# Kernel optimization log

Measured on AMD Instinct MI355X. Metric: run time of the kernel, lower is better.

The kernel has to match this reference:

```python
import jax, jax.numpy as jnp
import numpy as np

H = 2048
EPS = 1e-5

def _layernorm(x, g, b):
    mu = jnp.mean(x, axis=-1, keepdims=True)
    var = jnp.mean(jnp.square(x - mu), axis=-1, keepdims=True)
    return (x - mu) * jax.lax.rsqrt(var + EPS) * g + b

def setup_inputs() -> dict:
    key = jax.random.key(0)
    ks = jax.random.split(key, 12)
    s = 1.0 / np.sqrt(H)
    inp = {
        "x": jax.random.normal(ks[0], (2, 2048, H), dtype=jnp.float32),
        "ln1_g": jnp.ones((H,), jnp.float32),
        "ln1_b": jnp.zeros((H,), jnp.float32),
        "ln2_g": jnp.ones((H,), jnp.float32),
        "ln2_b": jnp.zeros((H,), jnp.float32),
        "qkv_w": jax.random.uniform(ks[1], (H, 3 * H), jnp.float32, -s, s),
        "qkv_b": jax.random.uniform(ks[2], (3 * H,), jnp.float32, -s, s),
        "out_w": jax.random.uniform(ks[3], (H, H), jnp.float32, -s, s),
        "out_b": jax.random.uniform(ks[4], (H,), jnp.float32, -s, s),
        "mlp_w1": jax.random.uniform(ks[5], (H, 4 * H), jnp.float32, -s, s),
        "mlp_b1": jax.random.uniform(ks[6], (4 * H,), jnp.float32, -s, s),
        "mlp_w2": jax.random.uniform(ks[7], (4 * H, H), jnp.float32, -1.0 / np.sqrt(4 * H), 1.0 / np.sqrt(4 * H)),
        "mlp_b2": jax.random.uniform(ks[8], (H,), jnp.float32, -1.0 / np.sqrt(4 * H), 1.0 / np.sqrt(4 * H)),
    }
    return inp

def reference(x, ln1_g, ln1_b, ln2_g, ln2_b, qkv_w, qkv_b, out_w, out_b, mlp_w1, mlp_b1, mlp_w2, mlp_b2):
    residual = x
    h = _layernorm(x, ln1_g, ln1_b)
    qkv = h @ qkv_w + qkv_b                      # [B,S,3H]
    q, k, v = jnp.split(qkv, 3, axis=-1)         # each [B,S,H] (single-head attention)
    scores = jnp.einsum('bsh,bth->bst', q, k) / jnp.sqrt(jnp.float32(H))
    attn = jax.nn.softmax(scores, axis=-1)
    attn_out = jnp.einsum('bst,bth->bsh', attn, v)
    attn_out = attn_out @ out_w + out_b
    x = residual + attn_out                      # dropout is identity in eval
    residual = x
    h = _layernorm(x, ln2_g, ln2_b)
    h = jax.nn.gelu(h @ mlp_w1 + mlp_b1, approximate=False)
    h = h @ mlp_w2 + mlp_b2
    return residual + h
```

## Files before the change

### kernel.cpp

```cpp
#include <hip/hip_runtime.h>
#include <hip/hip_bf16.h>
#include <math.h>

typedef __bf16 bf16_t;
typedef __bf16 bf16x8 __attribute__((ext_vector_type(8)));
typedef __bf16 bf16x4 __attribute__((ext_vector_type(4)));
typedef float  f32x4  __attribute__((ext_vector_type(4)));

enum { EPI_BF16_BIAS = 0, EPI_F32_SCALE = 1, EPI_BF16 = 2, EPI_F32_BIAS_RES = 3, EPI_BF16_BIAS_GELU = 4 };

__device__ __forceinline__ float gelu_exact(float v) {
  return 0.5f * v * (1.0f + erff(v * 0.7071067811865476f));
}

__device__ __forceinline__ void gld_lds16(const bf16_t* g, bf16_t* l) {
  __builtin_amdgcn_global_load_lds(
      (const __attribute__((address_space(1))) uint32_t*)(uintptr_t)g,
      (__attribute__((address_space(3))) uint32_t*)(uintptr_t)l, 16, 0, 0);
}

#define PH_BARRIER() do { __builtin_amdgcn_s_barrier(); __builtin_amdgcn_sched_barrier(0); } while(0)
#define LGKM0() do { asm volatile("s_waitcnt lgkmcnt(0)" ::: "memory"); __builtin_amdgcn_sched_barrier(0); } while(0)
#define VMCNT4() asm volatile("s_waitcnt vmcnt(4)" ::: "memory")
#define VMCNT0() asm volatile("s_waitcnt vmcnt(0)" ::: "memory")

#define RD(base, rowbase, ks) \
  (*(const bf16x8*)((base) + ((rowbase) + lr) * 64 + (((((ks) << 2) | lg)) ^ (lr & 7)) * 8))

#define DO_MFMA(IBASE, JBASE) \
  __builtin_amdgcn_s_setprio(1); \
  { _Pragma("unroll") for (int ii = 0; ii < 4; ++ii) \
    _Pragma("unroll") for (int jj = 0; jj < 2; ++jj) \
    _Pragma("unroll") for (int ks = 0; ks < 2; ++ks) \
      acc[(IBASE)+ii][(JBASE)+jj] = __builtin_amdgcn_mfma_f32_16x16x32_bf16( \
          aF[ii][ks], bF[jj][ks], acc[(IBASE)+ii][(JBASE)+jj], 0, 0, 0); } \
  __builtin_amdgcn_s_setprio(0);

template<int EPI>
__global__ __launch_bounds__(512, 2) void tb_gemm8(
    const bf16_t* __restrict__ A, int lda, long long strideA,
    const bf16_t* __restrict__ B, int ldb, long long strideB,
    const float* __restrict__ bias,
    const float* __restrict__ resid,
    void* __restrict__ Cp, int ldc, long long strideC,
    int K, float scale)
{
  __shared__ __align__(16) bf16_t sm[65536];

  const int tid = threadIdx.x;
  const int lane = tid & 63;
  const int wid = tid >> 6;
  const int wm = wid >> 2;
  const int wn = wid & 3;
  const int lr = lane & 15;
  const int lg = lane >> 4;
  const int z = blockIdx.z;
  const int m0 = blockIdx.y * 256;
  const int n0 = blockIdx.x * 256;

  const bf16_t* Ag = A + (size_t)z * strideA;
  const bf16_t* Bg = B + (size_t)z * strideB;

  const int l3 = lane >> 3;
  const int sl8 = ((lane & 7) ^ l3) << 3;

  f32x4 acc[8][4];
#pragma unroll
  for (int i = 0; i < 8; ++i)
#pragma unroll
    for (int j = 0; j < 4; ++j) acc[i][j] = (f32x4){0.f, 0.f, 0.f, 0.f};

  auto stage = [&](bf16_t* da, bf16_t* db, int kt, int H) {
#pragma unroll
    for (int q = 0; q < 2; ++q) {
      int c = (wid << 1) + q;
      int row = (H << 7) + (c << 3) + l3;
      gld_lds16(Ag + (size_t)(m0 + row) * lda + kt + sl8, da + (H << 13) + (c << 9) + lane * 8);
      gld_lds16(Bg + (size_t)(n0 + row) * ldb + kt + sl8, db + (H << 13) + (c << 9) + lane * 8);
    }
  };

  const int NT = K >> 6;
  stage(sm, sm + 16384, 0, 0);
  stage(sm, sm + 16384, 0, 1);

  bf16x8 aF[4][2], bF[2][2];

  for (int t = 0; t < NT; ++t) {
    bf16_t* cura = sm + ((t & 1) << 15);
    bf16_t* curb = cura + 16384;
    bf16_t* nxta = sm + (((t + 1) & 1) << 15);
    bf16_t* nxtb = nxta + 16384;
    const int ktn = (t + 1) << 6;
    const bool lastt = (t == NT - 1);

    VMCNT4();
    PH_BARRIER();
#pragma unroll
    for (int ii = 0; ii < 4; ++ii) {
      aF[ii][0] = RD(cura, ii * 32 + wm * 16, 0);
      aF[ii][1] = RD(cura, ii * 32 + wm * 16, 1);
    }
#pragma unroll
    for (int jj = 0; jj < 2; ++jj) {
      bF[jj][0] = RD(curb, jj * 64 + wn * 16, 0);
      bF[jj][1] = RD(curb, jj * 64 + wn * 16, 1);
    }
    if (!lastt) stage(nxta, nxtb, ktn, 0);
    LGKM0();
    DO_MFMA(0, 0);

    if (lastt) { VMCNT0(); } else { VMCNT4(); }
    PH_BARRIER();
#pragma unroll
    for (int jj = 0; jj < 2; ++jj) {
      bF[jj][0] = RD(curb, 128 + jj * 64 + wn * 16, 0);
      bF[jj][1] = RD(curb, 128 + jj * 64 + wn * 16, 1);
    }
    if (!lastt) stage(nxta, nxtb, ktn, 1);
    LGKM0();
    DO_MFMA(0, 2);

    PH_BARRIER();
#pragma unroll
    for (int ii = 0; ii < 4; ++ii) {
      aF[ii][0] = RD(cura, 128 + ii * 32 + wm * 16, 0);
      aF[ii][1] = RD(cura, 128 + ii * 32 + wm * 16, 1);
    }
    LGKM0();
    DO_MFMA(4, 2);

    PH_BARRIER();
#pragma unroll
    for (int jj = 0; jj < 2; ++jj) {
      bF[jj][0] = RD(curb, jj * 64 + wn * 16, 0);
      bF[jj][1] = RD(curb, jj * 64 + wn * 16, 1);
    }
    LGKM0();
    DO_MFMA(4, 0);
  }

#pragma unroll
  for (int i = 0; i < 8; ++i) {
    const int mr = ((i >> 2) << 7) + ((i & 3) << 5) + (wm << 4);
#pragma unroll
    for (int j = 0; j < 4; ++j) {
      const int nc = ((j >> 1) << 7) + ((j & 1) << 6) + (wn << 4);
#pragma unroll
      for (int r = 0; r < 4; ++r) {
        int row = m0 + mr + lg * 4 + r;
        int col = n0 + nc + lr;
        float v = acc[i][j][r] * scale;
        if constexpr (EPI == EPI_BF16_BIAS || EPI == EPI_F32_BIAS_RES || EPI == EPI_BF16_BIAS_GELU)
          v += bias[col];
        if constexpr (EPI == EPI_BF16_BIAS_GELU)
          v = gelu_exact(v);
        if constexpr (EPI == EPI_F32_BIAS_RES)
          v += resid[(size_t)row * ldc + col];
        if constexpr (EPI == EPI_BF16_BIAS || EPI == EPI_BF16 || EPI == EPI_BF16_BIAS_GELU) {
          ((bf16_t*)Cp)[(size_t)z * strideC + (size_t)row * ldc + col] = (bf16_t)v;
        } else {
          ((float*)Cp)[(size_t)z * strideC + (size_t)row * ldc + col] = v;
        }
      }
    }
  }
}

__global__ __launch_bounds__(256) void tb_transpose_cast(
    const float* __restrict__ in, bf16_t* __restrict__ outT, int R, int C)
{
  __shared__ float tile[32][33];
  int c0 = blockIdx.x * 32;
  int r0 = blockIdx.y * 32;
  int t = threadIdx.x;
  int r = t >> 3;
  int c4 = (t & 7) * 4;
  float4 d = *(const float4*)(in + (size_t)(r0 + r) * C + c0 + c4);
  tile[r][c4 + 0] = d.x; tile[r][c4 + 1] = d.y; tile[r][c4 + 2] = d.z; tile[r][c4 + 3] = d.w;
  __syncthreads();
  int c = t >> 3;
  int r4 = (t & 7) * 4;
  bf16x4 o;
  o[0] = (bf16_t)tile[r4 + 0][c];
  o[1] = (bf16_t)tile[r4 + 1][c];
  o[2] = (bf16_t)tile[r4 + 2][c];
  o[3] = (bf16_t)tile[r4 + 3][c];
  *(bf16x4*)(outT + (size_t)(c0 + c) * R + r0 + r4) = o;
}

__global__ __launch_bounds__(256) void tb_transpose_bf16(
    const bf16_t* __restrict__ in, int ldin, long long sIn,
    bf16_t* __restrict__ out, int ldout, long long sOut)
{
  __shared__ bf16_t tile[32][40];
  int z = blockIdx.z;
  const bf16_t* src = in + (size_t)z * sIn;
  bf16_t* dst = out + (size_t)z * sOut;
  int c0 = blockIdx.x * 32;
  int r0 = blockIdx.y * 32;
  int t = threadIdx.x;
  int r = t >> 3;
  int c4 = (t & 7) * 4;
  bf16x4 d = *(const bf16x4*)(src + (size_t)(r0 + r) * ldin + c0 + c4);
  *(bf16x4*)&tile[r][c4] = d;
  __syncthreads();
  int c = t >> 3;
  int r4 = (t & 7) * 4;
  bf16x4 o;
  o[0] = tile[r4 + 0][c];
  o[1] = tile[r4 + 1][c];
  o[2] = tile[r4 + 2][c];
  o[3] = tile[r4 + 3][c];
  *(bf16x4*)(dst + (size_t)(c0 + c) * ldout + r0 + r4) = o;
}

__global__ __launch_bounds__(256) void tb_layernorm(
    const float* __restrict__ x, const float* __restrict__ g, const float* __restrict__ b,
    bf16_t* __restrict__ h)
{
  __shared__ float sa[4], sb[4];
  int row = blockIdx.x;
  int t = threadIdx.x;
  const float* xr = x + (size_t)row * 2048;
  float4 v0 = *(const float4*)(xr + t * 8);
  float4 v1 = *(const float4*)(xr + t * 8 + 4);
  float a[8] = {v0.x, v0.y, v0.z, v0.w, v1.x, v1.y, v1.z, v1.w};
  float s = 0.f, q = 0.f;
#pragma unroll
  for (int j = 0; j < 8; ++j) { s += a[j]; q += a[j] * a[j]; }
#pragma unroll
  for (int o = 32; o; o >>= 1) { s += __shfl_down(s, o); q += __shfl_down(q, o); }
  int w = t >> 6, l = t & 63;
  if (l == 0) { sa[w] = s; sb[w] = q; }
  __syncthreads();
  if (t == 0) {
    sa[0] = sa[0] + sa[1] + sa[2] + sa[3];
    sb[0] = sb[0] + sb[1] + sb[2] + sb[3];
  }
  __syncthreads();
  float mu = sa[0] * (1.0f / 2048.0f);
  float var = sb[0] * (1.0f / 2048.0f) - mu * mu;
  float rs = rsqrtf(var + 1e-5f);
  float4 g0 = *(const float4*)(g + t * 8);
  float4 g1 = *(const float4*)(g + t * 8 + 4);
  float4 b0 = *(const float4*)(b + t * 8);
  float4 b1 = *(const float4*)(b + t * 8 + 4);
  float gv[8] = {g0.x, g0.y, g0.z, g0.w, g1.x, g1.y, g1.z, g1.w};
  float bv[8] = {b0.x, b0.y, b0.z, b0.w, b1.x, b1.y, b1.z, b1.w};
  bf16x8 o8;
#pragma unroll
  for (int j = 0; j < 8; ++j) o8[j] = (bf16_t)((a[j] - mu) * rs * gv[j] + bv[j]);
  *(bf16x8*)(h + (size_t)row * 2048 + t * 8) = o8;
}

__global__ __launch_bounds__(256) void tb_softmax(
    const float* __restrict__ S, bf16_t* __restrict__ P)
{
  __shared__ float sa[4];
  int row = blockIdx.x;
  int t = threadIdx.x;
  const float* sr = S + (size_t)row * 2048;
  float4 a0 = *(const float4*)(sr + t * 8);
  float4 a1 = *(const float4*)(sr + t * 8 + 4);
  float v[8] = {a0.x, a0.y, a0.z, a0.w, a1.x, a1.y, a1.z, a1.w};
  float m = v[0];
#pragma unroll
  for (int j = 1; j < 8; ++j) m = fmaxf(m, v[j]);
#pragma unroll
  for (int o = 32; o; o >>= 1) m = fmaxf(m, __shfl_down(m, o));
  int w = t >> 6, l = t & 63;
  if (l == 0) sa[w] = m;
  __syncthreads();
  if (t == 0) sa[0] = fmaxf(fmaxf(sa[0], sa[1]), fmaxf(sa[2], sa[3]));
  __syncthreads();
  m = sa[0];
  __syncthreads();
  float s = 0.f;
#pragma unroll
  for (int j = 0; j < 8; ++j) { v[j] = expf(v[j] - m); s += v[j]; }
#pragma unroll
  for (int o = 32; o; o >>= 1) s += __shfl_down(s, o);
  if (l == 0) sa[w] = s;
  __syncthreads();
  if (t == 0) sa[0] = sa[0] + sa[1] + sa[2] + sa[3];
  __syncthreads();
  float inv = 1.0f / sa[0];
  bf16x8 o8;
#pragma unroll
  for (int j = 0; j < 8; ++j) o8[j] = (bf16_t)(v[j] * inv);
  *(bf16x8*)(P + (size_t)row * 2048 + t * 8) = o8;
}

extern "C" void kernel_launch(void* const* d_in, const int* in_sizes, int n_in,
                              void* d_out, int out_size, void* d_ws, size_t ws_size,
                              hipStream_t stream) {
  const float* x     = (const float*)d_in[0];
  const float* ln1_g = (const float*)d_in[1];
  const float* ln1_b = (const float*)d_in[2];
  const float* ln2_g = (const float*)d_in[3];
  const float* ln2_b = (const float*)d_in[4];
  const float* qkv_w = (const float*)d_in[5];
  const float* qkv_b = (const float*)d_in[6];
  const float* out_w = (const float*)d_in[7];
  const float* out_b = (const float*)d_in[8];
  const float* w1    = (const float*)d_in[9];
  const float* b1    = (const float*)d_in[10];
  const float* w2    = (const float*)d_in[11];
  const float* b2    = (const float*)d_in[12];
  float* out = (float*)d_out;
  char* ws = (char*)d_ws;

  bf16_t* qkv_wT = (bf16_t*)(ws + 0);
  bf16_t* out_wT = (bf16_t*)(ws + 25165824);
  bf16_t* w1T    = (bf16_t*)(ws + 33554432);
  bf16_t* w2T    = (bf16_t*)(ws + 67108864);
  bf16_t* h_bf   = (bf16_t*)(ws + 100663296);
  bf16_t* qkv_bf = (bf16_t*)(ws + 117440512);
  float*  scores = (float*)(ws + 167772160);
  bf16_t* attn_bf= (bf16_t*)(ws + 201326592);
  bf16_t* ao_bf  = (bf16_t*)(ws + 218103808);
  float*  x2     = (float*)(ws + 234881024);
  bf16_t* mid_bf = (bf16_t*)(ws + 117440512);
  bf16_t* Vt     = (bf16_t*)(ws + 234881024);

  const float inv_sqrt_h = 0.022097086912079608f;

  tb_transpose_cast<<<dim3(6144 / 32, 2048 / 32), 256, 0, stream>>>(qkv_w, qkv_wT, 2048, 6144);
  tb_transpose_cast<<<dim3(2048 / 32, 2048 / 32), 256, 0, stream>>>(out_w, out_wT, 2048, 2048);
  tb_transpose_cast<<<dim3(8192 / 32, 2048 / 32), 256, 0, stream>>>(w1, w1T, 2048, 8192);
  tb_transpose_cast<<<dim3(2048 / 32, 8192 / 32), 256, 0, stream>>>(w2, w2T, 8192, 2048);

  tb_layernorm<<<4096, 256, 0, stream>>>(x, ln1_g, ln1_b, h_bf);

  tb_gemm8<EPI_BF16_BIAS><<<dim3(24, 16, 1), 512, 0, stream>>>(
      h_bf, 2048, 0, qkv_wT, 2048, 0, qkv_b, nullptr, qkv_bf, 6144, 0, 2048, 1.0f);

  tb_transpose_bf16<<<dim3(64, 64, 2), 256, 0, stream>>>(
      qkv_bf + 4096, 6144, 2048LL * 6144, Vt, 2048, 2048LL * 2048);

  tb_gemm8<EPI_F32_SCALE><<<dim3(8, 8, 2), 512, 0, stream>>>(
      qkv_bf, 6144, 2048LL * 6144, qkv_bf + 2048, 6144, 2048LL * 6144,
      nullptr, nullptr, scores, 2048, 2048LL * 2048, 2048, inv_sqrt_h);

  tb_softmax<<<4096, 256, 0, stream>>>(scores, attn_bf);

  tb_gemm8<EPI_BF16><<<dim3(8, 8, 2), 512, 0, stream>>>(
      attn_bf, 2048, 2048LL * 2048, Vt, 2048, 2048LL * 2048,
      nullptr, nullptr, ao_bf, 2048, 2048LL * 2048, 2048, 1.0f);

  tb_gemm8<EPI_F32_BIAS_RES><<<dim3(8, 16, 1), 512, 0, stream>>>(
      ao_bf, 2048, 0, out_wT, 2048, 0, out_b, x, x2, 2048, 0, 2048, 1.0f);

  tb_layernorm<<<4096, 256, 0, stream>>>(x2, ln2_g, ln2_b, h_bf);

  tb_gemm8<EPI_BF16_BIAS_GELU><<<dim3(32, 16, 1), 512, 0, stream>>>(
      h_bf, 2048, 0, w1T, 2048, 0, b1, nullptr, mid_bf, 8192, 0, 2048, 1.0f);

  tb_gemm8<EPI_F32_BIAS_RES><<<dim3(8, 16, 1), 512, 0, stream>>>(
      mid_bf, 8192, 0, w2T, 8192, 0, b2, x2, out, 2048, 0, 8192, 1.0f);
}
```

Baseline: 791.4 us.

## Re-pipeline GEMM staging per half-tile and split-K the MLP down projection

The GEMM main loop now issues the next tile's A and B halves separately, spread across the four MFMA phases. Each phase is bracketed by finer vmcnt/lgkmcnt waits and barriers, aiming for better overlap of global-to-LDS loads with compute. The final MLP GEMM, which launched only 128 blocks, is split along K into two partial fp32 outputs. A new elementwise kernel sums those partials with the bias and residual. This raises CU utilization at the cost of extra fp32 traffic, one more launch, and more barriers per iteration.

```diff
diff --git a/kernel.cpp b/kernel.cpp
--- a/kernel.cpp
+++ b/kernel.cpp
@@ -19,10 +19,10 @@
       (__attribute__((address_space(3))) uint32_t*)(uintptr_t)l, 16, 0, 0);
 }
 
-#define PH_BARRIER() do { __builtin_amdgcn_s_barrier(); __builtin_amdgcn_sched_barrier(0); } while(0)
+#define SB()    __builtin_amdgcn_s_barrier()
 #define LGKM0() do { asm volatile("s_waitcnt lgkmcnt(0)" ::: "memory"); __builtin_amdgcn_sched_barrier(0); } while(0)
-#define VMCNT4() asm volatile("s_waitcnt vmcnt(4)" ::: "memory")
-#define VMCNT0() asm volatile("s_waitcnt vmcnt(0)" ::: "memory")
+#define VMW(N)  asm volatile("s_waitcnt vmcnt(" #N ")" ::: "memory")
+#define LGKMW(N) asm volatile("s_waitcnt lgkmcnt(" #N ")" ::: "memory")
 
 #define RD(base, rowbase, ks) \
   (*(const bf16x8*)((base) + ((rowbase) + lr) * 64 + (((((ks) << 2) | lg)) ^ (lr & 7)) * 8))
@@ -58,8 +58,8 @@
   const int m0 = blockIdx.y * 256;
   const int n0 = blockIdx.x * 256;
 
-  const bf16_t* Ag = A + (size_t)z * strideA;
-  const bf16_t* Bg = B + (size_t)z * strideB;
+  const bf16_t* Ag = A + (size_t)z * strideA + (size_t)m0 * lda;
+  const bf16_t* Bg = B + (size_t)z * strideB + (size_t)n0 * ldb;
 
   const int l3 = lane >> 3;
   const int sl8 = ((lane & 7) ^ l3) << 3;
@@ -70,19 +70,22 @@
 #pragma unroll
     for (int j = 0; j < 4; ++j) acc[i][j] = (f32x4){0.f, 0.f, 0.f, 0.f};
 
-  auto stage = [&](bf16_t* da, bf16_t* db, int kt, int H) {
+  auto stageM = [&](const bf16_t* G, int ld, bf16_t* dst, int kt, int H) {
 #pragma unroll
     for (int q = 0; q < 2; ++q) {
       int c = (wid << 1) + q;
       int row = (H << 7) + (c << 3) + l3;
-      gld_lds16(Ag + (size_t)(m0 + row) * lda + kt + sl8, da + (H << 13) + (c << 9) + lane * 8);
-      gld_lds16(Bg + (size_t)(n0 + row) * ldb + kt + sl8, db + (H << 13) + (c << 9) + lane * 8);
+      gld_lds16(G + (size_t)row * ld + kt + sl8, dst + (H << 13) + (c << 9) + lane * 8);
     }
   };
 
   const int NT = K >> 6;
-  stage(sm, sm + 16384, 0, 0);
-  stage(sm, sm + 16384, 0, 1);
+  stageM(Ag, lda, sm, 0, 0);
+  stageM(Bg, ldb, sm + 16384, 0, 0);
+  stageM(Bg, ldb, sm + 16384, 0, 1);
+  stageM(Ag, lda, sm, 0, 1);
+  VMW(4);
+  SB();
 
   bf16x8 aF[4][2], bF[2][2];
 
@@ -92,10 +95,8 @@
     bf16_t* nxta = sm + (((t + 1) & 1) << 15);
     bf16_t* nxtb = nxta + 16384;
     const int ktn = (t + 1) << 6;
-    const bool lastt = (t == NT - 1);
-
-    VMCNT4();
-    PH_BARRIER();
+    const bool last = (t == NT - 1);
+
 #pragma unroll
     for (int ii = 0; ii < 4; ++ii) {
       aF[ii][0] = RD(cura, ii * 32 + wm * 16, 0);
@@ -106,38 +107,50 @@
       bF[jj][0] = RD(curb, jj * 64 + wn * 16, 0);
       bF[jj][1] = RD(curb, jj * 64 + wn * 16, 1);
     }
-    if (!lastt) stage(nxta, nxtb, ktn, 0);
+    if (!last) stageM(Ag, lda, nxta, ktn, 0);
+    if (last) { VMW(2); } else { VMW(4); }
+    LGKMW(8);
+    SB();
     LGKM0();
     DO_MFMA(0, 0);
-
-    if (lastt) { VMCNT0(); } else { VMCNT4(); }
-    PH_BARRIER();
+    SB();
+
 #pragma unroll
     for (int jj = 0; jj < 2; ++jj) {
       bF[jj][0] = RD(curb, 128 + jj * 64 + wn * 16, 0);
       bF[jj][1] = RD(curb, 128 + jj * 64 + wn * 16, 1);
     }
-    if (!lastt) stage(nxta, nxtb, ktn, 1);
+    if (!last) stageM(Bg, ldb, nxtb, ktn, 0);
+    if (last) { VMW(0); } else { VMW(4); }
+    SB();
     LGKM0();
     DO_MFMA(0, 2);
-
-    PH_BARRIER();
+    SB();
+
 #pragma unroll
     for (int ii = 0; ii < 4; ++ii) {
       aF[ii][0] = RD(cura, 128 + ii * 32 + wm * 16, 0);
       aF[ii][1] = RD(cura, 128 + ii * 32 + wm * 16, 1);
     }
+    if (!last) stageM(Bg, ldb, nxtb, ktn, 1);
+    SB();
     LGKM0();
     DO_MFMA(4, 2);
-
-    PH_BARRIER();
+    SB();
+
 #pragma unroll
     for (int jj = 0; jj < 2; ++jj) {
       bF[jj][0] = RD(curb, jj * 64 + wn * 16, 0);
       bF[jj][1] = RD(curb, jj * 64 + wn * 16, 1);
     }
+    if (!last) {
+      stageM(Ag, lda, nxta, ktn, 1);
+      VMW(4);
+    }
+    SB();
     LGKM0();
     DO_MFMA(4, 0);
+    SB();
   }
 
 #pragma unroll
@@ -165,6 +178,24 @@
       }
     }
   }
+}
+
+__global__ __launch_bounds__(256) void tb_combine(
+    const float* __restrict__ x2, const float* __restrict__ p0,
+    const float* __restrict__ p1, const float* __restrict__ bias,
+    float* __restrict__ out)
+{
+  size_t o = ((size_t)blockIdx.x * 256 + threadIdx.x) * 4;
+  float4 a = *(const float4*)(x2 + o);
+  float4 b = *(const float4*)(p0 + o);
+  float4 c = *(const float4*)(p1 + o);
+  float4 bb = *(const float4*)(bias + (o & 2047));
+  float4 r;
+  r.x = a.x + b.x + c.x + bb.x;
+  r.y = a.y + b.y + c.y + bb.y;
+  r.z = a.z + b.z + c.z + bb.z;
+  r.w = a.w + b.w + c.w + bb.w;
+  *(float4*)(out + o) = r;
 }
 
 __global__ __launch_bounds__(256) void tb_transpose_cast(
@@ -323,6 +354,8 @@
   float*  x2     = (float*)(ws + 234881024);
   bf16_t* mid_bf = (bf16_t*)(ws + 117440512);
   bf16_t* Vt     = (bf16_t*)(ws + 234881024);
+  float*  part0  = (float*)(ws + 0);
+  float*  part1  = (float*)(ws + 201326592);
 
   const float inv_sqrt_h = 0.022097086912079608f;
 
@@ -357,6 +390,9 @@
   tb_gemm8<EPI_BF16_BIAS_GELU><<<dim3(32, 16, 1), 512, 0, stream>>>(
       h_bf, 2048, 0, w1T, 2048, 0, b1, nullptr, mid_bf, 8192, 0, 2048, 1.0f);
 
-  tb_gemm8<EPI_F32_BIAS_RES><<<dim3(8, 16, 1), 512, 0, stream>>>(
-      mid_bf, 8192, 0, w2T, 8192, 0, b2, x2, out, 2048, 0, 8192, 1.0f);
-}
+  tb_gemm8<EPI_F32_SCALE><<<dim3(8, 16, 2), 512, 0, stream>>>(
+      mid_bf, 8192, 4096, w2T, 8192, 4096,
+      nullptr, nullptr, part0, 2048, 50331648LL, 4096, 1.0f);
+
+  tb_combine<<<8192, 256, 0, stream>>>(x2, part0, part1, b2, out);
+}
```

Result: faster. 745.7 us (-5.8%).
